# Kernel optimization log

Measured on AMD Instinct MI355X. Metric: run time of the kernel, lower is better.

The kernel has to match this reference:

```python
import jax, jax.numpy as jnp
import numpy as np

DN = ('NCDHW', 'OIDHW', 'NCDHW')


def conv3d(x, w, b, stride=2, pad=1):
    # w: [Cout, Cin, k, k, k] (PyTorch Conv3d layout == OIDHW)
    y = jax.lax.conv_general_dilated(x, w, (stride,) * 3, [(pad, pad)] * 3,
                                     dimension_numbers=DN)
    return y + b[None, :, None, None, None]


def convT3d(x, w, b, stride=2, pad=1):
    # w: [Cin, Cout, k, k, k] (PyTorch ConvTranspose3d layout).
    # ConvTranspose(k,s,p) == conv(lhs_dilated by s, flipped kernel, pad = k-1-p)
    k = w.shape[2]
    wf = jnp.transpose(jnp.flip(w, (2, 3, 4)), (1, 0, 2, 3, 4))  # -> OIDHW
    p = k - 1 - pad
    y = jax.lax.conv_general_dilated(x, wf, (1, 1, 1), [(p, p)] * 3,
                                     lhs_dilation=(stride,) * 3,
                                     dimension_numbers=DN)
    return y + b[None, :, None, None, None]


def setup_inputs() -> dict:
    key = jax.random.key(0)
    ks = jax.random.split(key, 14)
    s = 0.05
    inp = {
        'x': jax.random.normal(ks[0], (4, 1, 128, 128, 128), jnp.float32),
        # encoder conv weights (OIDHW) + biases
        'w1': jax.random.normal(ks[1], (16, 1, 4, 4, 4), jnp.float32) * s,
        'b1': jnp.zeros((16,), jnp.float32),
        'w2': jax.random.normal(ks[2], (32, 16, 4, 4, 4), jnp.float32) * s,
        'b2': jnp.zeros((32,), jnp.float32),
        'w3': jax.random.normal(ks[3], (64, 32, 4, 4, 4), jnp.float32) * s,
        'b3': jnp.zeros((64,), jnp.float32),
        # VQ codebook [num_embeddings=512, latent_dim=64]
        'codebook': jax.random.normal(ks[4], (512, 64), jnp.float32),
        # decoder conv-transpose weights (PyTorch layout: [Cin, Cout, k,k,k]) + biases
        'dw1': jax.random.normal(ks[5], (64, 32, 4, 4, 4), jnp.float32) * s,
        'db1': jnp.zeros((32,), jnp.float32),
        'dw2': jax.random.normal(ks[6], (32, 16, 4, 4, 4), jnp.float32) * s,
        'db2': jnp.zeros((16,), jnp.float32),
        'dw3': jax.random.normal(ks[7], (16, 1, 4, 4, 4), jnp.float32) * s,
        'db3': jnp.zeros((1,), jnp.float32),
    }
    return inp


def reference(x, w1, b1, w2, b2, w3, b3, codebook, dw1, db1, dw2, db2, dw3, db3):
    # ---- encoder ----
    h = jax.nn.relu(conv3d(x, w1, b1))
    h = jax.nn.relu(conv3d(h, w2, b2))
    z_e = conv3d(h, w3, b3)                      # [B, C=64, D, H, W]
    B, C, D, H, W = z_e.shape

    # ---- vector quantization (cdist + argmin + gather) ----
    zf = jnp.transpose(z_e.reshape(B, C, -1), (0, 2, 1))   # [B, N, C]
    # squared euclidean distances (argmin identical to cdist argmin)
    d2 = (jnp.sum(zf * zf, axis=-1, keepdims=True)
          + jnp.sum(codebook * codebook, axis=-1)[None, None, :]
          - 2.0 * jnp.einsum('bnc,kc->bnk', zf, codebook))  # [B, N, K]
    encoding_indices = jnp.argmin(d2, axis=-1)              # [B, N]
    q = codebook[encoding_indices]                          # [B, N, C]
    quantized = jnp.transpose(q, (0, 2, 1)).reshape(B, C, D, H, W)
    # straight-through estimator
    quantized = z_e + jax.lax.stop_gradient(quantized - z_e)

    # ---- decoder ----
    h = jax.nn.relu(convT3d(quantized, dw1, db1))
    h = jax.nn.relu(convT3d(h, dw2, db2))
    x_hat = jax.nn.sigmoid(convT3d(h, dw3, db3))
    return (x_hat, quantized, z_e)
```

## Files before the change

kernel.cpp:

```cpp
#include <hip/hip_runtime.h>
#include <math.h>


__device__ __forceinline__ float4 ld4(const float* p) {
  float4 q; __builtin_memcpy(&q, p, 16); return q;
}
struct F3 { float x, y, z; };
__device__ __forceinline__ F3 ld3(const float* p) {
  F3 q; __builtin_memcpy(&q, p, 12); return q;
}

#define WAVES_HINT __attribute__((amdgpu_waves_per_eu(2, 4)))

template<int CIN, int COUT>
__global__ __launch_bounds__(256) void k_repackT(const float* __restrict__ w,
                                                 float* __restrict__ dst) {
  const int idx = blockIdx.x * 256 + threadIdx.x;
  if (idx >= CIN * 8 * COUT * 8) return;
  const int a  = idx & 7;
  const int co = (idx >> 3) % COUT;
  const int p  = ((idx >> 3) / COUT) & 7;
  const int ci2 = idx / (8 * COUT * 8);
  const int az = a >> 2, ay = (a >> 1) & 1, ax = a & 1;
  const int pz = p >> 2, py = (p >> 1) & 1, px = p & 1;
  const int kz = 3 - pz - 2 * az, ky = 3 - py - 2 * ay, kx = 3 - px - 2 * ax;
  dst[(((size_t)(ci2 * 8 + p) * COUT + co) * 16) + az * 8 + (ay * 2 + ax)] =
      w[((size_t)ci2 * COUT + co) * 64 + (kz * 16 + ky * 4 + kx)];
}

template<int S, int D, int NCH>
__global__ __launch_bounds__(256) void k_zhalo(float* __restrict__ buf) {
  const int vol = S * S * S;
  const long long idx = (long long)blockIdx.x * 256 + threadIdx.x;
  if (idx >= (long long)NCH * vol) return;
  const int r = (int)(idx % vol);
  const int z = r / (S * S), y = (r / S) % S, x = r % S;
  if (z < 1 || z > D || y < 1 || y > D || x < 1 || x > D) buf[idx] = 0.0f;
}

template<int CIN, int COUT, int DIN, int DOUT, int OCG, int TZ, bool RELU,
         bool INP, int SIN, bool OUTP, int SOUT, int NG>
__global__ __launch_bounds__(256) WAVES_HINT
void k_conv(const float* __restrict__ xin, const float* __restrict__ wg,
            const float* __restrict__ bias, float* __restrict__ out) {
  constexpr int NBX = DOUT / 8, NBY = DOUT / 8, NBZ = DOUT / (4 * TZ);
  constexpr size_t VIN  = INP  ? (size_t)SIN * SIN * SIN : (size_t)DIN * DIN * DIN;
  constexpr size_t VOUT = OUTP ? (size_t)SOUT * SOUT * SOUT : (size_t)DOUT * DOUT * DOUT;
  const int tid = threadIdx.x;
  const int tx = tid & 7, ty = (tid >> 3) & 7, tz = tid >> 6;
  int bb = blockIdx.x;
  const int g  = bb % NG;  bb /= NG;
  const int gx = bb % NBX; bb /= NBX;
  const int gy = bb % NBY; bb /= NBY;
  const int gz = bb % NBZ; bb /= NBZ;
  const int b = bb;
  const int oc0 = g * OCG;
  const int ow = gx * 8 + tx, oh = gy * 8 + ty, od0 = gz * (4 * TZ) + tz;

  float acc[TZ][OCG];
#pragma unroll
  for (int j = 0; j < TZ; ++j)
#pragma unroll
    for (int c = 0; c < OCG; ++c) acc[j][c] = 0.0f;

#pragma unroll 1
  for (int ci = 0; ci < CIN; ++ci) {
    const float* xb = xin + (size_t)(b * CIN + ci) * VIN;
#pragma unroll 1
    for (int t16 = 0; t16 < 16; ++t16) {
      float4 q[TZ];
      if (INP) {
        const int zp = od0 * 2 + (t16 >> 2);
        const int yp = oh * 2 + (t16 & 3);
        const float* r0 = xb + ((size_t)zp * SIN + yp) * SIN + ow * 2;
#pragma unroll
        for (int j = 0; j < TZ; ++j) q[j] = ld4(r0 + (size_t)j * 8 * SIN * SIN);
      } else {
        const int y  = oh * 2 - 1 + (t16 & 3);
        const int x0 = ow * 2 - 1;
        const bool vy = (unsigned)y < (unsigned)DIN;
#pragma unroll
        for (int j = 0; j < TZ; ++j) {
          const int z = od0 * 2 - 1 + (t16 >> 2) + j * 8;
          const bool vz = vy && ((unsigned)z < (unsigned)DIN);
          const float* xr = xb + ((size_t)z * DIN + y) * DIN + x0;
          q[j].x = (vz && (unsigned)(x0 + 0) < (unsigned)DIN) ? xr[0] : 0.0f;
          q[j].y = (vz && (unsigned)(x0 + 1) < (unsigned)DIN) ? xr[1] : 0.0f;
          q[j].z = (vz && (unsigned)(x0 + 2) < (unsigned)DIN) ? xr[2] : 0.0f;
          q[j].w = (vz && (unsigned)(x0 + 3) < (unsigned)DIN) ? xr[3] : 0.0f;
        }
      }
#pragma unroll
      for (int c = 0; c < OCG; ++c) {
        const float4 w4 = ld4(wg + ((size_t)(oc0 + c) * CIN + ci) * 64 + t16 * 4);
#pragma unroll
        for (int j = 0; j < TZ; ++j) {
          acc[j][c] = fmaf(q[j].x, w4.x, acc[j][c]);
          acc[j][c] = fmaf(q[j].y, w4.y, acc[j][c]);
          acc[j][c] = fmaf(q[j].z, w4.z, acc[j][c]);
          acc[j][c] = fmaf(q[j].w, w4.w, acc[j][c]);
        }
      }
    }
  }

#pragma unroll
  for (int c = 0; c < OCG; ++c) {
    const float bv = bias[oc0 + c];
#pragma unroll
    for (int j = 0; j < TZ; ++j) {
      float v = acc[j][c] + bv;
      if (RELU) v = fmaxf(v, 0.0f);
      const int od = od0 + j * 4;
      if (OUTP)
        out[(size_t)(b * COUT + oc0 + c) * VOUT
            + ((size_t)(od + 1) * SOUT + (oh + 1)) * SOUT + (ow + 1)] = v;
      else
        out[(size_t)(b * COUT + oc0 + c) * VOUT
            + ((size_t)od * DOUT + oh) * DOUT + ow] = v;
    }
  }
}

template<int CIN, int COUT, int DIN, int OCG, int TZ, int EPI, int SIN,
         bool OUTP, int SOUT, int NG>
__global__ __launch_bounds__(256) WAVES_HINT
void k_convt(const float* __restrict__ xin, const float* __restrict__ wp,
             const float* __restrict__ bias, float* __restrict__ out) {
  constexpr int DOUT = 2 * DIN, NBX = DIN / 8, NBY = DIN / 8,
                NBZ = DIN / (4 * TZ);
  constexpr size_t VIN  = (size_t)SIN * SIN * SIN;
  constexpr size_t VOUT = OUTP ? (size_t)SOUT * SOUT * SOUT
                               : (size_t)DOUT * DOUT * DOUT;
  const int tid = threadIdx.x;
  const int tx = tid & 7, ty = (tid >> 3) & 7, tz = tid >> 6;
  int bb = blockIdx.x;
  const int g  = bb % NG;  bb /= NG;
  const int gx = bb % NBX; bb /= NBX;
  const int gy = bb % NBY; bb /= NBY;
  const int gz = bb % NBZ; bb /= NBZ;
  const int b = bb;
  const int oc0 = g * OCG;
  const int mx = gx * 8 + tx, my = gy * 8 + ty;
  const int mz0 = gz * (4 * TZ) + tz * TZ;

  float acc[TZ][8][OCG];
#pragma unroll
  for (int j = 0; j < TZ; ++j)
#pragma unroll
    for (int p = 0; p < 8; ++p)
#pragma unroll
      for (int c = 0; c < OCG; ++c) acc[j][p][c] = 0.0f;

#pragma unroll 1
  for (int ci = 0; ci < CIN; ++ci) {
    const float* xb = xin + (size_t)(b * CIN + ci) * VIN
                          + ((size_t)mz0 * SIN + my) * SIN + mx;
    float xn[TZ + 2][3][3];
#pragma unroll
    for (int dz = 0; dz < TZ + 2; ++dz)
#pragma unroll
      for (int dy = 0; dy < 3; ++dy) {
        const F3 t = ld3(xb + ((size_t)dz * SIN + dy) * SIN);
        xn[dz][dy][0] = t.x; xn[dz][dy][1] = t.y; xn[dz][dy][2] = t.z;
      }
    const float* wci = wp + (size_t)ci * 8 * COUT * 16;
#pragma unroll
    for (int p = 0; p < 8; ++p) {
      const int pz = p >> 2, py = (p >> 1) & 1, px = p & 1;
#pragma unroll
      for (int c = 0; c < OCG; ++c) {
        const float* wb = wci + ((size_t)p * COUT + (oc0 + c)) * 16;
        const float4 wA = ld4(wb);
        const float4 wB = ld4(wb + 8);
#pragma unroll
        for (int j = 0; j < TZ; ++j) {
          acc[j][p][c] = fmaf(xn[j + pz    ][py    ][px    ], wA.x, acc[j][p][c]);
          acc[j][p][c] = fmaf(xn[j + pz    ][py    ][px + 1], wA.y, acc[j][p][c]);
          acc[j][p][c] = fmaf(xn[j + pz    ][py + 1][px    ], wA.z, acc[j][p][c]);
          acc[j][p][c] = fmaf(xn[j + pz    ][py + 1][px + 1], wA.w, acc[j][p][c]);
          acc[j][p][c] = fmaf(xn[j + pz + 1][py    ][px    ], wB.x, acc[j][p][c]);
          acc[j][p][c] = fmaf(xn[j + pz + 1][py    ][px + 1], wB.y, acc[j][p][c]);
          acc[j][p][c] = fmaf(xn[j + pz + 1][py + 1][px    ], wB.z, acc[j][p][c]);
          acc[j][p][c] = fmaf(xn[j + pz + 1][py + 1][px + 1], wB.w, acc[j][p][c]);
        }
      }
    }
  }

#pragma unroll
  for (int c = 0; c < OCG; ++c) {
    const float bv = bias[oc0 + c];
#pragma unroll
    for (int j = 0; j < TZ; ++j) {
      const int mz = mz0 + j;
#pragma unroll
      for (int p = 0; p < 8; ++p) {
        const int pz = p >> 2, py = (p >> 1) & 1, px = p & 1;
        float v = acc[j][p][c] + bv;
        if (EPI == 1) v = fmaxf(v, 0.0f);
        if (EPI == 2) v = 1.0f / (1.0f + expf(-v));
        if (OUTP)
          out[(size_t)(b * COUT + oc0 + c) * VOUT
              + ((size_t)(2 * mz + pz + 1) * SOUT + (2 * my + py + 1)) * SOUT
              + (2 * mx + px + 1)] = v;
        else
          out[(size_t)(b * COUT + oc0 + c) * VOUT
              + ((size_t)(2 * mz + pz) * DOUT + (2 * my + py)) * DOUT
              + (2 * mx + px)] = v;
      }
    }
  }
}

__global__ __launch_bounds__(256) void k_vq(const float* __restrict__ ze,
                                            const float* __restrict__ cb,
                                            float* __restrict__ quant,
                                            float* __restrict__ quantp) {
  __shared__ float ct[64 * 65];
  __shared__ float zs[4][64];
  __shared__ int   bis[4];
  const int tid  = threadIdx.x;
  const int lane = tid & 63;
  const int wv   = tid >> 6;
  const int p0 = blockIdx.x * 4;
  const int b  = p0 >> 12;
  const int n0 = p0 & 4095;

  {
    const int c = tid >> 2, j = tid & 3;
    zs[j][c] = ze[((size_t)(b * 64 + c) << 12) + n0 + j];
  }

  float best = 3.4e38f;
  int bi = 0;
#pragma unroll 1
  for (int ch = 0; ch < 8; ++ch) {
    __syncthreads();
    for (int i = tid; i < 4096; i += 256) {
      const int r = i >> 6, c = i & 63;
      ct[r * 65 + c] = cb[((ch * 64 + r) << 6) + c];
    }
    __syncthreads();
    float d = 0.0f;
#pragma unroll 8
    for (int c = 0; c < 64; ++c) {
      const float t = zs[wv][c] - ct[lane * 65 + c];
      d = fmaf(t, t, d);
    }
    const int k = ch * 64 + lane;
    if (d < best) { best = d; bi = k; }
  }
#pragma unroll
  for (int off = 32; off > 0; off >>= 1) {
    const float ob = __shfl_down(best, off);
    const int   oi = __shfl_down(bi, off);
    if (ob < best || (ob == best && oi < bi)) { best = ob; bi = oi; }
  }
  if (lane == 0) bis[wv] = bi;
  __syncthreads();
  {
    const int c = tid >> 2, j = tid & 3;
    const float val = cb[(bis[j] << 6) + c];
    const int n = n0 + j;
    quant[((size_t)(b * 64 + c) << 12) + n] = val;
    const int zz = n >> 8, yy = (n >> 4) & 15, xx = n & 15;
    quantp[(size_t)(b * 64 + c) * 8000
           + ((size_t)(zz + 1) * 20 + (yy + 1)) * 20 + (xx + 1)] = val;
  }
}

extern "C" void kernel_launch(void* const* d_in, const int* in_sizes, int n_in,
                              void* d_out, int out_size, void* d_ws, size_t ws_size,
                              hipStream_t stream) {
  const float* x   = (const float*)d_in[0];
  const float* w1  = (const float*)d_in[1];
  const float* b1  = (const float*)d_in[2];
  const float* w2  = (const float*)d_in[3];
  const float* b2  = (const float*)d_in[4];
  const float* w3  = (const float*)d_in[5];
  const float* b3  = (const float*)d_in[6];
  const float* cb  = (const float*)d_in[7];
  const float* dw1 = (const float*)d_in[8];
  const float* db1 = (const float*)d_in[9];
  const float* dw2 = (const float*)d_in[10];
  const float* db2 = (const float*)d_in[11];
  const float* dw3 = (const float*)d_in[12];
  const float* db3 = (const float*)d_in[13];

  float* outf  = (float*)d_out;
  float* xhat  = outf;
  float* quant = outf + 8388608;
  float* ze    = outf + 9437184;

  float* regA = (float*)d_ws;
  float* regB = regA + (size_t)64 * 68 * 68 * 68;
  float* regC = regB + (size_t)128 * 36 * 36 * 36;
  float* t1p = regC + (size_t)256 * 20 * 20 * 20;
  float* t2p = t1p + 262144;
  float* t3p = t2p + 65536;

  k_repackT<64, 32><<<512, 256, 0, stream>>>(dw1, t1p);
  k_repackT<32, 16><<<128, 256, 0, stream>>>(dw2, t2p);
  k_repackT<16, 1><<<4, 256, 0, stream>>>(dw3, t3p);
  k_zhalo<68, 64, 64><<<78608, 256, 0, stream>>>(regA);
  k_zhalo<36, 32, 128><<<23328, 256, 0, stream>>>(regB);
  k_zhalo<20, 16, 256><<<8000, 256, 0, stream>>>(regC);

  k_conv<1, 16, 128, 64, 16, 2, true, false, 0, true, 68, 1>
      <<<2048, 256, 0, stream>>>(x, w1, b1, regA);
  k_conv<16, 32, 64, 32, 16, 1, true, true, 68, true, 36, 2>
      <<<1024, 256, 0, stream>>>(regA, w2, b2, regB);
  k_conv<32, 64, 32, 16, 4, 1, false, true, 36, false, 16, 16>
      <<<1024, 256, 0, stream>>>(regB, w3, b3, ze);
  k_vq<<<4096, 256, 0, stream>>>(ze, cb, quant, regC);
  k_convt<64, 32, 16, 2, 1, 1, 20, true, 36, 16>
      <<<1024, 256, 0, stream>>>(regC, t1p, db1, regB);
  k_convt<32, 16, 32, 2, 4, 1, 36, true, 68, 8>
      <<<1024, 256, 0, stream>>>(regB, t2p, db2, regA);
  k_convt<16, 1, 64, 1, 4, 2, 68, false, 0, 1>
      <<<1024, 256, 0, stream>>>(regA, t3p, db3, xhat);
}
```

Baseline: 1.089 ms.

## Stage convT input halo tiles in double-buffered LDS with register prefetch

The transposed-conv kernel now cooperatively loads each input channel's halo tile for the block into shared memory. The next channel's tile is prefetched into registers during compute and written to the other LDS buffer afterwards. Each thread then reads its 3x3 neighbourhoods from LDS instead of issuing overlapping global loads. This removes redundant global traffic across neighbouring threads, at the cost of two barriers per channel, extra registers for the prefetch and added LDS use that may lower occupancy.

```diff
diff --git a/kernel.cpp b/kernel.cpp
--- a/kernel.cpp
+++ b/kernel.cpp
@@ -129,9 +129,13 @@
              const float* __restrict__ bias, float* __restrict__ out) {
   constexpr int DOUT = 2 * DIN, NBX = DIN / 8, NBY = DIN / 8,
                 NBZ = DIN / (4 * TZ);
+  constexpr int ZT  = 4 * TZ + 2;
+  constexpr int NEL = ZT * 10 * 10;
+  constexpr int NR  = (NEL + 255) / 256;
   constexpr size_t VIN  = (size_t)SIN * SIN * SIN;
   constexpr size_t VOUT = OUTP ? (size_t)SOUT * SOUT * SOUT
                                : (size_t)DOUT * DOUT * DOUT;
+  __shared__ float lds[2][ZT][10][12];
   const int tid = threadIdx.x;
   const int tx = tid & 7, ty = (tid >> 3) & 7, tz = tid >> 6;
   int bb = blockIdx.x;
@@ -144,6 +148,19 @@
   const int mx = gx * 8 + tx, my = gy * 8 + ty;
   const int mz0 = gz * (4 * TZ) + tz * TZ;
 
+  int goff[NR], loff[NR];
+#pragma unroll
+  for (int r = 0; r < NR; ++r) {
+    const int e  = tid + 256 * r;
+    const int ez = e / 100, rem = e - ez * 100;
+    const int ey = rem / 10, ex = rem - ey * 10;
+    goff[r] = (ez * SIN + ey) * SIN + ex;
+    loff[r] = (ez * 10 + ey) * 12 + ex;
+  }
+  const float* xt0 = xin + (size_t)b * CIN * VIN
+                   + ((size_t)(gz * (4 * TZ)) * SIN + gy * 8) * SIN + gx * 8;
+  float* ldsf = &lds[0][0][0][0];
+
   float acc[TZ][8][OCG];
 #pragma unroll
   for (int j = 0; j < TZ; ++j)
@@ -151,19 +168,42 @@
     for (int p = 0; p < 8; ++p)
 #pragma unroll
       for (int c = 0; c < OCG; ++c) acc[j][p][c] = 0.0f;
+
+  {
+    float rg[NR];
+#pragma unroll
+    for (int r = 0; r < NR; ++r)
+      if (tid + 256 * r < NEL) rg[r] = xt0[goff[r]];
+#pragma unroll
+    for (int r = 0; r < NR; ++r)
+      if (tid + 256 * r < NEL) ldsf[loff[r]] = rg[r];
+  }
+  __syncthreads();
 
 #pragma unroll 1
   for (int ci = 0; ci < CIN; ++ci) {
-    const float* xb = xin + (size_t)(b * CIN + ci) * VIN
-                          + ((size_t)mz0 * SIN + my) * SIN + mx;
+    float rg[NR];
+    const bool pf = (ci + 1 < CIN);
+    if (pf) {
+      const float* xc = xt0 + (size_t)(ci + 1) * VIN;
+#pragma unroll
+      for (int r = 0; r < NR; ++r)
+        if (tid + 256 * r < NEL) rg[r] = xc[goff[r]];
+    }
+
+    const int cur = ci & 1;
+    const float* Lb = ldsf + cur * (ZT * 120);
     float xn[TZ + 2][3][3];
 #pragma unroll
     for (int dz = 0; dz < TZ + 2; ++dz)
 #pragma unroll
       for (int dy = 0; dy < 3; ++dy) {
-        const F3 t = ld3(xb + ((size_t)dz * SIN + dy) * SIN);
-        xn[dz][dy][0] = t.x; xn[dz][dy][1] = t.y; xn[dz][dy][2] = t.z;
-      }
+        const float* rrow = Lb + ((tz * TZ + dz) * 10 + (ty + dy)) * 12 + tx;
+        xn[dz][dy][0] = rrow[0];
+        xn[dz][dy][1] = rrow[1];
+        xn[dz][dy][2] = rrow[2];
+      }
+
     const float* wci = wp + (size_t)ci * 8 * COUT * 16;
 #pragma unroll
     for (int p = 0; p < 8; ++p) {
@@ -186,6 +226,15 @@
         }
       }
     }
+
+    __syncthreads();
+    if (pf) {
+      float* Ln = ldsf + (cur ^ 1) * (ZT * 120);
+#pragma unroll
+      for (int r = 0; r < NR; ++r)
+        if (tid + 256 * r < NEL) Ln[loff[r]] = rg[r];
+    }
+    __syncthreads();
   }
 
 #pragma unroll
```

After: 1.154 ms. 6.0% more time.
